# Kernel tuning notes

Hardware: AMD Instinct MI355X
Metric: run time of the kernel (lower is better)

The kernel has to match this reference:

```python
import jax, jax.numpy as jnp
import numpy as np

B, S, D, H = 4, 2048, 1024, 16
DK = D // H
THETA = 10000.0


def _rope(x, pos):
    # x: [..., S, DK]; interleaved-pair rotation as in the torch module
    dk = x.shape[-1]
    inv_freq = 1.0 / (THETA ** (jnp.arange(0, dk, 2, dtype=jnp.float32) / dk))  # [dk/2]
    freqs = pos.astype(jnp.float32)[:, None] * inv_freq  # [S, dk/2]
    cos, sin = jnp.cos(freqs), jnp.sin(freqs)
    xr = x.reshape(*x.shape[:-1], dk // 2, 2)
    x0, x1 = xr[..., 0], xr[..., 1]
    rot = jnp.stack([x0 * cos - x1 * sin, x0 * sin + x1 * cos], axis=-1)
    return rot.reshape(x.shape)


def setup_inputs() -> dict:
    key = jax.random.key(0)
    ks = jax.random.split(key, 5)
    scale = 0.02
    return {
        "x": jax.random.normal(ks[0], (B, S, D), dtype=jnp.float32),
        "Wq": jax.random.normal(ks[1], (D, D), dtype=jnp.float32) * scale,
        "Wk": jax.random.normal(ks[2], (D, D), dtype=jnp.float32) * scale,
        "Wv": jax.random.normal(ks[3], (D, D), dtype=jnp.float32) * scale,
        "Wo": jax.random.normal(ks[4], (D, D), dtype=jnp.float32) * scale,
    }


def reference(x, Wq, Wk, Wv, Wo):
    b, s, d = x.shape
    pos = jnp.arange(s)
    # projections (Linear with no bias, y = x @ W^T)
    q = jnp.einsum('bsd,ed->bse', x, Wq).reshape(b, s, H, DK).transpose(0, 2, 1, 3)
    k = jnp.einsum('bsd,ed->bse', x, Wk).reshape(b, s, H, DK).transpose(0, 2, 1, 3)
    v = jnp.einsum('bsd,ed->bse', x, Wv).reshape(b, s, H, DK).transpose(0, 2, 1, 3)
    q = _rope(q, pos)
    k = _rope(k, pos)
    scores = jnp.einsum('bhqd,bhkd->bhqk', q, k) / jnp.sqrt(jnp.float32(DK))
    causal = jnp.tril(jnp.ones((s, s), dtype=bool))
    scores = jnp.where(causal, scores, -jnp.inf)
    attn = jax.nn.softmax(scores, axis=-1)
    out = jnp.einsum('bhqk,bhkd->bhqd', attn, v)
    out = out.transpose(0, 2, 1, 3).reshape(b, s, d)
    return jnp.einsum('bsd,ed->bse', out, Wo)
```

## Files before the change

kernel.cpp:

```cpp
#include <hip/hip_runtime.h>

#define B_  4
#define S_  2048
#define D_  1024
#define H_  16
#define DK_ 64
#define BH_ (B_*H_)
#define L2E 1.44269504088896f

typedef __attribute__((ext_vector_type(8))) short bf16x8;
typedef __attribute__((ext_vector_type(4))) float f32x4;
typedef __attribute__((ext_vector_type(16))) float f32x16;
typedef __attribute__((ext_vector_type(4))) unsigned u32x4;
typedef unsigned short u16;

__device__ __forceinline__ u16 f2bf(float f){
  unsigned u = __builtin_bit_cast(unsigned, f);
  u += 0x7fffu + ((u >> 16) & 1u);
  return (u16)(u >> 16);
}
__device__ __forceinline__ float bf2f(u16 h){
  unsigned u = ((unsigned)h) << 16;
  return __builtin_bit_cast(float, u);
}

#define GLD16(g,l) __builtin_amdgcn_global_load_lds( \
    (const __attribute__((address_space(1))) void*)(g), \
    (__attribute__((address_space(3))) void*)(l), 16, 0, 0)

#define MFMA16(a,b,c) __builtin_amdgcn_mfma_f32_16x16x32_bf16((a),(b),(c),0,0,0)
#define MFMA32(a,b,c) __builtin_amdgcn_mfma_f32_32x32x16_bf16((a),(b),(c),0,0,0)

__global__ void cast_kernel(const float4* __restrict__ in, ushort4* __restrict__ out, int n4){
  int i = blockIdx.x*blockDim.x + threadIdx.x;
  int stride = gridDim.x*blockDim.x;
  for (; i < n4; i += stride){
    float4 v = in[i];
    ushort4 o;
    o.x = f2bf(v.x); o.y = f2bf(v.y); o.z = f2bf(v.z); o.w = f2bf(v.w);
    out[i] = o;
  }
}

__global__ void cast4_kernel(const float4* __restrict__ w0, const float4* __restrict__ w1,
                             const float4* __restrict__ w2, const float4* __restrict__ w3,
                             ushort4* __restrict__ out){
  const int per = D_*D_/4;
  int i = blockIdx.x*blockDim.x + threadIdx.x;
  int stride = gridDim.x*blockDim.x;
  for (; i < 4*per; i += stride){
    int m = i / per, r = i - m*per;
    const float4* src = (m==0)?w0:(m==1)?w1:(m==2)?w2:w3;
    float4 v = src[r];
    ushort4 o;
    o.x = f2bf(v.x); o.y = f2bf(v.y); o.z = f2bf(v.z); o.w = f2bf(v.w);
    out[i] = o;
  }
}

__global__ void trig_kernel(float* __restrict__ ct, float* __restrict__ st){
  int t = blockIdx.x*blockDim.x + threadIdx.x;
  int i = t & 31, s = t >> 5;
  float expo = -(float)(2*i) * (1.0f/(float)DK_);
  float inv = powf(10000.0f, expo);
  float ang = (float)s * inv;
  ct[t] = cosf(ang);
  st[t] = sinf(ang);
}

template<int MODE>
__global__ __launch_bounds__(256, 2)
void gemm_bt(const u16* __restrict__ A,
             const u16* __restrict__ B0, const u16* __restrict__ B1, const u16* __restrict__ B2,
             u16* __restrict__ O0, u16* __restrict__ O1, u16* __restrict__ O2,
             float* __restrict__ Cf,
             const float* __restrict__ ct, const float* __restrict__ st, int K){
  __shared__ __align__(16) u16 lds[32768];

  const int id = (int)blockIdx.x;
  const int nchunk = (MODE==0) ? 192 : 64;
  const int swz = (id & 7)*nchunk + (id >> 3);
  int z = 0, rem = swz;
  if (MODE == 0){ z = swz >> 9; rem = swz & 511; }
  const int m0 = (rem >> 3) * 128, n0 = (rem & 7) * 128;

  const u16* Bm = B0;
  u16* Om = O0;
  if (MODE == 0){
    if (z == 1){ Bm = B1; Om = O1; }
    else if (z == 2){ Bm = B2; Om = O2; }
  }
  const int tid = threadIdx.x, wave = tid>>6, lane = tid&63;
  const int wm = wave>>1, wn = wave&1;
  const int srow = lane>>3, scol = (lane&7)*8;

  f32x4 acc[4][4];
  #pragma unroll
  for (int m=0;m<4;++m)
    #pragma unroll
    for (int n=0;n<4;++n) acc[m][n] = (f32x4){0.f,0.f,0.f,0.f};

  #define STAGE(kk0,b) { \
    u16* sA = lds + (b)*16384; \
    u16* sB = sA + 8192; \
    _Pragma("unroll") \
    for (int j=0;j<4;++j){ \
      int rb = (wave*4 + j)*8; \
      GLD16(A  + (size_t)(m0 + rb + srow)*K + (kk0) + scol, sA + rb*64); \
      GLD16(Bm + (size_t)(n0 + rb + srow)*K + (kk0) + scol, sB + rb*64); \
    } }

  STAGE(0, 0);
  __syncthreads();

  int cur = 0;
  #pragma unroll 1
  for (int k0 = 0; k0 < K; k0 += 64){
    if (k0 + 64 < K) STAGE(k0 + 64, cur^1);
    const u16* lA = lds + cur*16384;
    const u16* lB = lA + 8192;
    #pragma unroll
    for (int kk=0;kk<2;++kk){
      bf16x8 af[4], bfr[4];
      #pragma unroll
      for (int m=0;m<4;++m) af[m]  = *(const bf16x8*)&lA[(wm*64 + m*16 + (lane&15))*64 + kk*32 + (lane>>4)*8];
      #pragma unroll
      for (int n=0;n<4;++n) bfr[n] = *(const bf16x8*)&lB[(wn*64 + n*16 + (lane&15))*64 + kk*32 + (lane>>4)*8];
      #pragma unroll
      for (int m=0;m<4;++m)
        #pragma unroll
        for (int n=0;n<4;++n)
          acc[m][n] = MFMA16(af[m], bfr[n], acc[m][n]);
    }
    __syncthreads();
    cur ^= 1;
  }
  #undef STAGE

  if (MODE == 0 && z != 2){
    const float scale = (z == 0) ? 0.125f : 1.0f;
    #pragma unroll
    for (int m=0;m<4;++m){
      const int lr0 = wm*64 + m*16 + ((lane>>4)<<2);
      #pragma unroll
      for (int n=0;n<4;++n){
        const int lc = wn*64 + n*16 + (lane&15);
        #pragma unroll
        for (int r=0;r<4;++r){
          const int lr = lr0 + r;
          lds[lr*128 + (lc ^ (((lr>>2)&7)<<4))] = f2bf(acc[m][n][r]);
        }
      }
    }
    __syncthreads();
    #pragma unroll
    for (int k=0;k<8;++k){
      const int cid = k*256 + tid;
      const int rr = cid >> 4, cc = cid & 15;
      bf16x8 v = *(const bf16x8*)&lds[rr*128 + ((cc*8) ^ (((rr>>2)&7)<<4))];
      const int i = m0 + rr, bb = i >> 11, s = i & (S_-1);
      const int e0 = n0 + cc*8, h = e0 >> 6, dk0 = e0 & 63;
      const float4 c4 = *(const float4*)(ct + s*32 + (dk0>>1));
      const float4 s4 = *(const float4*)(st + s*32 + (dk0>>1));
      const float cc4[4] = {c4.x,c4.y,c4.z,c4.w};
      const float ss4[4] = {s4.x,s4.y,s4.z,s4.w};
      bf16x8 o;
      #pragma unroll
      for (int j=0;j<4;++j){
        const float x0 = bf2f((u16)v[2*j]);
        const float x1 = bf2f((u16)v[2*j+1]);
        o[2*j]   = (short)f2bf((x0*cc4[j] - x1*ss4[j])*scale);
        o[2*j+1] = (short)f2bf((x0*ss4[j] + x1*cc4[j])*scale);
      }
      *(bf16x8*)(Om + ((size_t)((bb*H_ + h)*S_ + s))*DK_ + dk0) = o;
    }
  } else {
    #pragma unroll
    for (int m=0;m<4;++m){
      const int rb = m0 + wm*64 + m*16 + ((lane>>4)<<2);
      #pragma unroll
      for (int n=0;n<4;++n){
        const int e = n0 + wn*64 + n*16 + (lane&15);
        if (MODE == 0){
          const int h = e>>6, dk = e&63;
          const int b = rb >> 11, s0 = rb & (S_-1);
          ushort4 w4;
          w4.x = f2bf(acc[m][n][0]); w4.y = f2bf(acc[m][n][1]);
          w4.z = f2bf(acc[m][n][2]); w4.w = f2bf(acc[m][n][3]);
          *(ushort4*)(Om + ((size_t)((b*H_ + h)*DK_ + dk))*S_ + s0) = w4;
        } else {
          #pragma unroll
          for (int r=0;r<4;++r)
            Cf[(size_t)(rb + r)*D_ + e] = acc[m][n][r];
        }
      }
    }
  }
}

__global__ __launch_bounds__(256, 4)
void attn_kernel(const u16* __restrict__ Q, const u16* __restrict__ K,
                 const u16* __restrict__ Vt, u16* __restrict__ O){
  __shared__ __align__(16) u16 lK[2][64*64];
  __shared__ __align__(16) u16 lV[2][64*64];

  const int bh = blockIdx.x;
  const int qt = (int)(gridDim.y - 1 - blockIdx.y);
  const int b = bh >> 4, h = bh & 15;
  const int tid = threadIdx.x, wave = tid>>6, lane = tid&63;
  const int hi = lane >> 5, l31 = lane & 31;
  const int q0 = qt*128, qw = q0 + wave*32;
  const int qg = qw + l31;
  const u16* Qb = Q  + (size_t)bh*S_*DK_;
  const u16* Kb = K  + (size_t)bh*S_*DK_;
  const u16* Vb = Vt + (size_t)bh*DK_*S_;

  bf16x8 qf[4];
  #pragma unroll
  for (int ds=0; ds<4; ++ds)
    qf[ds] = *(const bf16x8*)(Qb + (size_t)qg*DK_ + ds*16 + hi*8);

  f32x16 oacc[2];
  oacc[0] = (f32x16)0.f; oacc[1] = (f32x16)0.f;
  float m_run = -1e30f, l_run = 0.f;

  const int srow8 = lane >> 3;
  const int csw = ((lane&7) ^ srow8) << 3;

  const int kv_end = (qt+1)*128;

  #pragma unroll
  for (int it=0; it<2; ++it){
    const int rb = (it*4 + wave)*8;
    const int row = rb + srow8;
    GLD16(Kb + (size_t)row*DK_ + csw, lK[0] + rb*64);
    GLD16(Vb + (size_t)row*S_ + csw,  lV[0] + rb*64);
  }
  __syncthreads();

  int cur = 0;
  for (int kv0 = 0; kv0 < kv_end; kv0 += 64){
    const int nxt = kv0 + 64;
    if (nxt < kv_end){
      #pragma unroll
      for (int it=0; it<2; ++it){
        const int rb = (it*4 + wave)*8;
        const int row = rb + srow8;
        GLD16(Kb + (size_t)(nxt+row)*DK_ + csw, lK[cur^1] + rb*64);
        GLD16(Vb + (size_t)row*S_ + nxt + csw,  lV[cur^1] + rb*64);
      }
    }

    if (kv0 < qw + 32){
      f32x16 sacc[2];
      sacc[0] = (f32x16)0.f; sacc[1] = (f32x16)0.f;
      __builtin_amdgcn_s_setprio(1);
      #pragma unroll
      for (int kb=0; kb<2; ++kb){
        const int krow = kb*32 + l31;
        #pragma unroll
        for (int ds=0; ds<4; ++ds){
          bf16x8 kf = *(const bf16x8*)&lK[cur][krow*64 + (((ds*2+hi) ^ (krow&7))<<3)];
          sacc[kb] = MFMA32(kf, qf[ds], sacc[kb]);
        }
      }
      __builtin_amdgcn_s_setprio(0);

      if (kv0 + 63 > qw){
        #pragma unroll
        for (int kb=0; kb<2; ++kb)
          #pragma unroll
          for (int r=0; r<16; ++r){
            const int kvg = kv0 + kb*32 + 4*hi + (r&3) + 8*(r>>2);
            if (kvg > qg) sacc[kb][r] = -1e30f;
          }
      }

      float mx = sacc[0][0];
      #pragma unroll
      for (int r=1; r<16; ++r) mx = fmaxf(mx, sacc[0][r]);
      #pragma unroll
      for (int r=0; r<16; ++r) mx = fmaxf(mx, sacc[1][r]);
      mx = fmaxf(mx, __shfl_xor(mx, 32));
      if (!__all((mx - m_run)*L2E <= 8.0f)){
        const float mn = fmaxf(m_run, mx);
        const float alpha = exp2f((m_run - mn)*L2E);
        m_run = mn;
        l_run *= alpha;
        oacc[0] *= alpha;
        oacc[1] *= alpha;
      }
      const float nc = m_run * L2E;
      float ps = 0.f;
      #pragma unroll
      for (int kb=0; kb<2; ++kb)
        #pragma unroll
        for (int r=0; r<16; ++r){
          float v = exp2f(__builtin_fmaf(sacc[kb][r], L2E, -nc));
          sacc[kb][r] = v;
          ps += v;
        }
      ps += __shfl_xor(ps, 32);
      l_run += ps;

      bf16x8 pa[4];
      #pragma unroll
      for (int kb=0; kb<2; ++kb){
        unsigned w[8];
        #pragma unroll
        for (int i=0; i<8; ++i){
          float a = sacc[kb][2*i], b2 = sacc[kb][2*i+1];
          asm("v_cvt_pk_bf16_f32 %0, %1, %2" : "=v"(w[i]) : "v"(a), "v"(b2));
        }
        auto s02 = __builtin_amdgcn_permlane32_swap(w[0], w[2], false, false);
        auto s13 = __builtin_amdgcn_permlane32_swap(w[1], w[3], false, false);
        auto s46 = __builtin_amdgcn_permlane32_swap(w[4], w[6], false, false);
        auto s57 = __builtin_amdgcn_permlane32_swap(w[5], w[7], false, false);
        u32x4 ua = {s02[0], s13[0], s02[1], s13[1]};
        u32x4 ub = {s46[0], s57[0], s46[1], s57[1]};
        pa[kb*2+0] = __builtin_bit_cast(bf16x8, ua);
        pa[kb*2+1] = __builtin_bit_cast(bf16x8, ub);
      }

      __builtin_amdgcn_s_setprio(1);
      #pragma unroll
      for (int dkb=0; dkb<2; ++dkb){
        const int vrow = dkb*32 + l31;
        #pragma unroll
        for (int ks=0; ks<4; ++ks){
          bf16x8 vf = *(const bf16x8*)&lV[cur][vrow*64 + (((ks*2+hi) ^ (vrow&7))<<3)];
          oacc[dkb] = MFMA32(vf, pa[ks], oacc[dkb]);
        }
      }
      __builtin_amdgcn_s_setprio(0);
    }
    __syncthreads();
    cur ^= 1;
  }

  const float inv = 1.0f / l_run;
  #pragma unroll
  for (int dkb=0; dkb<2; ++dkb)
    #pragma unroll
    for (int rq=0; rq<4; ++rq){
      ushort4 w4;
      w4.x = f2bf(oacc[dkb][rq*4+0]*inv);
      w4.y = f2bf(oacc[dkb][rq*4+1]*inv);
      w4.z = f2bf(oacc[dkb][rq*4+2]*inv);
      w4.w = f2bf(oacc[dkb][rq*4+3]*inv);
      const int dk0 = dkb*32 + 8*rq + 4*hi;
      *(ushort4*)(O + (size_t)(b*S_+qg)*D_ + h*DK_ + dk0) = w4;
    }
}

extern "C" void kernel_launch(void* const* d_in, const int* in_sizes, int n_in,
                              void* d_out, int out_size, void* d_ws, size_t ws_size,
                              hipStream_t stream){
  const float* x  = (const float*)d_in[0];
  const float* Wq = (const float*)d_in[1];
  const float* Wk = (const float*)d_in[2];
  const float* Wv = (const float*)d_in[3];
  const float* Wo = (const float*)d_in[4];
  float* out = (float*)d_out;
  char* ws = (char*)d_ws;

  size_t off = 0;
  u16* xb  = (u16*)(ws + off); off += (size_t)B_*S_*D_*2;
  u16* wqb = (u16*)(ws + off); off += (size_t)D_*D_*2;
  u16* wkb = (u16*)(ws + off); off += (size_t)D_*D_*2;
  u16* wvb = (u16*)(ws + off); off += (size_t)D_*D_*2;
  u16* wob = (u16*)(ws + off); off += (size_t)D_*D_*2;
  u16* Qb  = (u16*)(ws + off); off += (size_t)BH_*S_*DK_*2;
  u16* Kb  = (u16*)(ws + off); off += (size_t)BH_*S_*DK_*2;
  u16* Vtb = (u16*)(ws + off); off += (size_t)BH_*S_*DK_*2;
  u16* Ob  = (u16*)(ws + off); off += (size_t)B_*S_*D_*2;
  float* ct = (float*)(ws + off); off += (size_t)S_*32*4;
  float* st = (float*)(ws + off); off += (size_t)S_*32*4;

  cast_kernel<<<2048,256,0,stream>>>((const float4*)x,  (ushort4*)xb,  B_*S_*D_/4);
  cast4_kernel<<<1024,256,0,stream>>>((const float4*)Wq, (const float4*)Wk,
                                      (const float4*)Wv, (const float4*)Wo, (ushort4*)wqb);
  trig_kernel<<<(S_*32)/256,256,0,stream>>>(ct, st);

  gemm_bt<0><<<1536,256,0,stream>>>(xb, wqb,wkb,wvb, Qb,Kb,Vtb, nullptr, ct, st, D_);

  attn_kernel<<<dim3(BH_, S_/128),256,0,stream>>>(Qb, Kb, Vtb, Ob);

  gemm_bt<1><<<512,256,0,stream>>>(Ob, wob,wob,wob, nullptr,nullptr,nullptr, out, nullptr, nullptr, D_);
}
```

Measured before the change: 185.0 us.

## Use 256x256-tile 8-wave QKV GEMM with quarter-step LDS pipelining

Replaces the QKV projection GEMM with a dedicated 512-thread kernel that computes 256x256 output tiles. It splits each K-step into four quadrant MFMA phases, interleaving global-to-LDS staging with explicit barriers, waitcnts and priority hints, and uses an XOR-swizzled LDS layout. The goal is more data reuse per tile, fewer LDS bank conflicts, and load latency hidden behind MFMA work. In exchange it uses 128KB of LDS and a large accumulator set, which lowers occupancy, and it adds a hand-tuned synchronisation scheme. The output GEMM is split into its own non-templated kernel.

```diff
diff --git a/kernel.cpp b/kernel.cpp
--- a/kernel.cpp
+++ b/kernel.cpp
@@ -30,6 +30,11 @@
 
 #define MFMA16(a,b,c) __builtin_amdgcn_mfma_f32_16x16x32_bf16((a),(b),(c),0,0,0)
 #define MFMA32(a,b,c) __builtin_amdgcn_mfma_f32_32x32x16_bf16((a),(b),(c),0,0,0)
+
+#define BARR() __builtin_amdgcn_s_barrier()
+#define LGKM0() do { asm volatile("s_waitcnt lgkmcnt(0)" ::: "memory"); \
+                     __builtin_amdgcn_sched_barrier(0); } while(0)
+#define VMW(N) asm volatile("s_waitcnt vmcnt(" #N ")" ::: "memory")
 
 __global__ void cast_kernel(const float4* __restrict__ in, ushort4* __restrict__ out, int n4){
   int i = blockIdx.x*blockDim.x + threadIdx.x;
@@ -68,28 +73,191 @@
   st[t] = sinf(ang);
 }
 
-template<int MODE>
+__global__ __launch_bounds__(512, 2)
+void gemm_qkv8(const u16* __restrict__ A,
+               const u16* __restrict__ B0m, const u16* __restrict__ B1m, const u16* __restrict__ B2m,
+               u16* __restrict__ O0, u16* __restrict__ O1, u16* __restrict__ O2,
+               const float* __restrict__ ct, const float* __restrict__ st){
+  __shared__ __align__(16) u16 lds[65536];
+
+  const int id = (int)blockIdx.x;
+  const int swz = (id & 7)*48 + (id >> 3);
+  const int z = swz >> 7;
+  const int rem = swz & 127;
+  const int m0 = (rem >> 2)*256, n0 = (rem & 3)*256;
+
+  const u16* Bm = (z==0) ? B0m : (z==1) ? B1m : B2m;
+  u16* Om = (z==0) ? O0 : (z==1) ? O1 : O2;
+
+  const int tid = threadIdx.x, wave = tid>>6, lane = tid&63;
+  const int wm = wave>>2, wn = wave&3;
+  const int l15 = lane & 15, l4 = lane >> 4;
+  const int srow8 = lane >> 3;
+  const int csw = ((lane&7) ^ srow8) << 3;
+
+  f32x4 acc[8][4];
+  #pragma unroll
+  for (int mi=0;mi<8;++mi)
+    #pragma unroll
+    for (int ni=0;ni<4;++ni) acc[mi][ni] = (f32x4){0.f,0.f,0.f,0.f};
+
+  #define STAGE_A(pp, mh, kc) do { \
+    u16* base_ = lds + (pp) + (mh)*8192; \
+    _Pragma("unroll") \
+    for (int j_=0;j_<2;++j_){ \
+      const int lr_ = (wave*2 + j_)*8; \
+      const int q_ = lr_ >> 6; \
+      const size_t grow_ = (size_t)(m0 + q_*128 + (mh)*64 + (lr_ & 63) + srow8); \
+      GLD16(A + grow_*1024 + (kc) + csw, base_ + lr_*64); \
+    } } while(0)
+
+  #define STAGE_B(pp, nh, kc) do { \
+    u16* base_ = lds + (pp) + 16384 + (nh)*8192; \
+    _Pragma("unroll") \
+    for (int j_=0;j_<2;++j_){ \
+      const int lr_ = (wave*2 + j_)*8; \
+      const int sub_ = lr_ >> 5; \
+      const size_t grow_ = (size_t)(n0 + sub_*64 + (nh)*32 + (lr_ & 31) + srow8); \
+      GLD16(Bm + grow_*1024 + (kc) + csw, base_ + lr_*64); \
+    } } while(0)
+
+  bf16x8 af[4][2], bfr[2][2];
+  #define LOAD_AF(pp, mh) do { \
+    const u16* ab_ = lds + (pp) + (mh)*8192; \
+    _Pragma("unroll") \
+    for (int m_=0;m_<4;++m_) \
+      _Pragma("unroll") \
+      for (int kk_=0;kk_<2;++kk_){ \
+        const int lr_ = wm*64 + m_*16 + l15; \
+        af[m_][kk_] = *(const bf16x8*)&ab_[lr_*64 + (((kk_*4 + l4) ^ (lr_&7))<<3)]; \
+      } } while(0)
+
+  #define LOAD_BF(pp, nh) do { \
+    const u16* bb_ = lds + (pp) + 16384 + (nh)*8192; \
+    _Pragma("unroll") \
+    for (int n_=0;n_<2;++n_) \
+      _Pragma("unroll") \
+      for (int kk_=0;kk_<2;++kk_){ \
+        const int lr_ = wn*32 + n_*16 + l15; \
+        bfr[n_][kk_] = *(const bf16x8*)&bb_[lr_*64 + (((kk_*4 + l4) ^ (lr_&7))<<3)]; \
+      } } while(0)
+
+  #define MFMAQ(mh, nh) do { \
+    _Pragma("unroll") \
+    for (int m_=0;m_<4;++m_) \
+      _Pragma("unroll") \
+      for (int n_=0;n_<2;++n_) \
+        _Pragma("unroll") \
+        for (int kk_=0;kk_<2;++kk_) \
+          acc[(mh)*4+m_][(nh)*2+n_] = MFMA16(af[m_][kk_], bfr[n_][kk_], acc[(mh)*4+m_][(nh)*2+n_]); \
+    } while(0)
+
+  STAGE_A(0, 0, 0); STAGE_A(0, 1, 0); STAGE_B(0, 0, 0); STAGE_B(0, 1, 0);
+  STAGE_B(32768, 0, 64); STAGE_A(32768, 1, 64);
+  VMW(4);
+  BARR();
+
+  #pragma unroll 1
+  for (int t = 0; t < 16; ++t){
+    const int p = (t & 1) << 15;
+    const int o = p ^ 32768;
+    const int kc1 = ((t+1 < 16) ? t+1 : 15)*64;
+    const int kc2 = ((t+2 < 16) ? t+2 : 15)*64;
+    LOAD_AF(p, 0); LOAD_BF(p, 0);
+    STAGE_A(o, 0, kc1);
+    BARR(); LGKM0();
+    __builtin_amdgcn_s_setprio(1); MFMAQ(0, 0); __builtin_amdgcn_s_setprio(0);
+    BARR();
+    LOAD_AF(p, 1);
+    STAGE_B(o, 1, kc1);
+    BARR(); LGKM0();
+    __builtin_amdgcn_s_setprio(1); MFMAQ(1, 0); __builtin_amdgcn_s_setprio(0);
+    BARR();
+    LOAD_BF(p, 1);
+    STAGE_B(p, 0, kc2);
+    BARR(); LGKM0();
+    __builtin_amdgcn_s_setprio(1); MFMAQ(1, 1); __builtin_amdgcn_s_setprio(0);
+    BARR();
+    LOAD_AF(p, 0);
+    STAGE_A(p, 1, kc2);
+    BARR(); LGKM0();
+    __builtin_amdgcn_s_setprio(1); MFMAQ(0, 1); __builtin_amdgcn_s_setprio(0);
+    VMW(4);
+    BARR();
+  }
+  #undef STAGE_A
+  #undef STAGE_B
+  #undef LOAD_AF
+  #undef LOAD_BF
+  #undef MFMAQ
+
+  VMW(0);
+  BARR();
+
+  if (z != 2){
+    const float scale = (z == 0) ? 0.125f : 1.0f;
+    #pragma unroll
+    for (int mi=0;mi<8;++mi){
+      const int rr0 = wm*128 + (mi>>2)*64 + (mi&3)*16 + l4*4;
+      #pragma unroll
+      for (int ni=0;ni<4;++ni){
+        const int cc = wn*64 + (ni>>1)*32 + (ni&1)*16 + l15;
+        #pragma unroll
+        for (int r=0;r<4;++r){
+          const int rr = rr0 + r;
+          lds[rr*256 + (((((cc>>3) ^ (rr&7)))<<3) | (cc&7))] = f2bf(acc[mi][ni][r]);
+        }
+      }
+    }
+    __syncthreads();
+    #pragma unroll
+    for (int k=0;k<16;++k){
+      const int cid = k*512 + tid;
+      const int rr = cid >> 5, cc8 = cid & 31;
+      bf16x8 v = *(const bf16x8*)&lds[rr*256 + ((cc8 ^ (rr&7))<<3)];
+      const int i = m0 + rr, bb = i >> 11, s = i & (S_-1);
+      const int e0 = n0 + cc8*8, h = e0 >> 6, dk0 = e0 & 63;
+      const float4 c4 = *(const float4*)(ct + s*32 + (dk0>>1));
+      const float4 s4 = *(const float4*)(st + s*32 + (dk0>>1));
+      const float cc4[4] = {c4.x,c4.y,c4.z,c4.w};
+      const float ss4[4] = {s4.x,s4.y,s4.z,s4.w};
+      bf16x8 o;
+      #pragma unroll
+      for (int j=0;j<4;++j){
+        const float x0 = bf2f((u16)v[2*j]);
+        const float x1 = bf2f((u16)v[2*j+1]);
+        o[2*j]   = (short)f2bf((x0*cc4[j] - x1*ss4[j])*scale);
+        o[2*j+1] = (short)f2bf((x0*ss4[j] + x1*cc4[j])*scale);
+      }
+      *(bf16x8*)(Om + ((size_t)((bb*H_ + h)*S_ + s))*DK_ + dk0) = o;
+    }
+  } else {
+    #pragma unroll
+    for (int mi=0;mi<8;++mi){
+      const int rb = m0 + wm*128 + (mi>>2)*64 + (mi&3)*16 + l4*4;
+      const int b = rb >> 11, s0 = rb & (S_-1);
+      #pragma unroll
+      for (int ni=0;ni<4;++ni){
+        const int e = n0 + wn*64 + (ni>>1)*32 + (ni&1)*16 + l15;
+        const int h = e>>6, dk = e&63;
+        ushort4 w4;
+        w4.x = f2bf(acc[mi][ni][0]); w4.y = f2bf(acc[mi][ni][1]);
+        w4.z = f2bf(acc[mi][ni][2]); w4.w = f2bf(acc[mi][ni][3]);
+        *(ushort4*)(Om + ((size_t)((b*H_ + h)*DK_ + dk))*S_ + s0) = w4;
+      }
+    }
+  }
+}
+
 __global__ __launch_bounds__(256, 2)
-void gemm_bt(const u16* __restrict__ A,
-             const u16* __restrict__ B0, const u16* __restrict__ B1, const u16* __restrict__ B2,
-             u16* __restrict__ O0, u16* __restrict__ O1, u16* __restrict__ O2,
-             float* __restrict__ Cf,
-             const float* __restrict__ ct, const float* __restrict__ st, int K){
+void gemm_out(const u16* __restrict__ A, const u16* __restrict__ Bw,
+              float* __restrict__ Cf){
   __shared__ __align__(16) u16 lds[32768];
 
   const int id = (int)blockIdx.x;
-  const int nchunk = (MODE==0) ? 192 : 64;
-  const int swz = (id & 7)*nchunk + (id >> 3);
-  int z = 0, rem = swz;
-  if (MODE == 0){ z = swz >> 9; rem = swz & 511; }
-  const int m0 = (rem >> 3) * 128, n0 = (rem & 7) * 128;
-
-  const u16* Bm = B0;
-  u16* Om = O0;
-  if (MODE == 0){
-    if (z == 1){ Bm = B1; Om = O1; }
-    else if (z == 2){ Bm = B2; Om = O2; }
-  }
+  const int swz = (id & 7)*64 + (id >> 3);
+  const int m0 = (swz >> 3) * 128, n0 = (swz & 7) * 128;
+
   const int tid = threadIdx.x, wave = tid>>6, lane = tid&63;
   const int wm = wave>>1, wn = wave&1;
   const int srow = lane>>3, scol = (lane&7)*8;
@@ -106,8 +274,8 @@
     _Pragma("unroll") \
     for (int j=0;j<4;++j){ \
       int rb = (wave*4 + j)*8; \
-      GLD16(A  + (size_t)(m0 + rb + srow)*K + (kk0) + scol, sA + rb*64); \
-      GLD16(Bm + (size_t)(n0 + rb + srow)*K + (kk0) + scol, sB + rb*64); \
+      GLD16(A  + (size_t)(m0 + rb + srow)*D_ + (kk0) + scol, sA + rb*64); \
+      GLD16(Bw + (size_t)(n0 + rb + srow)*D_ + (kk0) + scol, sB + rb*64); \
     } }
 
   STAGE(0, 0);
@@ -115,8 +283,8 @@
 
   int cur = 0;
   #pragma unroll 1
-  for (int k0 = 0; k0 < K; k0 += 64){
-    if (k0 + 64 < K) STAGE(k0 + 64, cur^1);
+  for (int k0 = 0; k0 < D_; k0 += 64){
+    if (k0 + 64 < D_) STAGE(k0 + 64, cur^1);
     const u16* lA = lds + cur*16384;
     const u16* lB = lA + 8192;
     #pragma unroll
@@ -137,63 +305,15 @@
   }
   #undef STAGE
 
-  if (MODE == 0 && z != 2){
-    const float scale = (z == 0) ? 0.125f : 1.0f;
-    #pragma unroll
-    for (int m=0;m<4;++m){
-      const int lr0 = wm*64 + m*16 + ((lane>>4)<<2);
-      #pragma unroll
-      for (int n=0;n<4;++n){
-        const int lc = wn*64 + n*16 + (lane&15);
-        #pragma unroll
-        for (int r=0;r<4;++r){
-          const int lr = lr0 + r;
-          lds[lr*128 + (lc ^ (((lr>>2)&7)<<4))] = f2bf(acc[m][n][r]);
-        }
-      }
-    }
-    __syncthreads();
-    #pragma unroll
-    for (int k=0;k<8;++k){
-      const int cid = k*256 + tid;
-      const int rr = cid >> 4, cc = cid & 15;
-      bf16x8 v = *(const bf16x8*)&lds[rr*128 + ((cc*8) ^ (((rr>>2)&7)<<4))];
-      const int i = m0 + rr, bb = i >> 11, s = i & (S_-1);
-      const int e0 = n0 + cc*8, h = e0 >> 6, dk0 = e0 & 63;
-      const float4 c4 = *(const float4*)(ct + s*32 + (dk0>>1));
-      const float4 s4 = *(const float4*)(st + s*32 + (dk0>>1));
-      const float cc4[4] = {c4.x,c4.y,c4.z,c4.w};
-      const float ss4[4] = {s4.x,s4.y,s4.z,s4.w};
-      bf16x8 o;
-      #pragma unroll
-      for (int j=0;j<4;++j){
-        const float x0 = bf2f((u16)v[2*j]);
-        const float x1 = bf2f((u16)v[2*j+1]);
-        o[2*j]   = (short)f2bf((x0*cc4[j] - x1*ss4[j])*scale);
-        o[2*j+1] = (short)f2bf((x0*ss4[j] + x1*cc4[j])*scale);
-      }
-      *(bf16x8*)(Om + ((size_t)((bb*H_ + h)*S_ + s))*DK_ + dk0) = o;
-    }
-  } else {
-    #pragma unroll
-    for (int m=0;m<4;++m){
-      const int rb = m0 + wm*64 + m*16 + ((lane>>4)<<2);
-      #pragma unroll
-      for (int n=0;n<4;++n){
-        const int e = n0 + wn*64 + n*16 + (lane&15);
-        if (MODE == 0){
-          const int h = e>>6, dk = e&63;
-          const int b = rb >> 11, s0 = rb & (S_-1);
-          ushort4 w4;
-          w4.x = f2bf(acc[m][n][0]); w4.y = f2bf(acc[m][n][1]);
-          w4.z = f2bf(acc[m][n][2]); w4.w = f2bf(acc[m][n][3]);
-          *(ushort4*)(Om + ((size_t)((b*H_ + h)*DK_ + dk))*S_ + s0) = w4;
-        } else {
-          #pragma unroll
-          for (int r=0;r<4;++r)
-            Cf[(size_t)(rb + r)*D_ + e] = acc[m][n][r];
-        }
-      }
+  #pragma unroll
+  for (int m=0;m<4;++m){
+    const int rb = m0 + wm*64 + m*16 + ((lane>>4)<<2);
+    #pragma unroll
+    for (int n=0;n<4;++n){
+      const int e = n0 + wn*64 + n*16 + (lane&15);
+      #pragma unroll
+      for (int r=0;r<4;++r)
+        Cf[(size_t)(rb + r)*D_ + e] = acc[m][n][r];
     }
   }
 }
@@ -382,9 +502,9 @@
                                       (const float4*)Wv, (const float4*)Wo, (ushort4*)wqb);
   trig_kernel<<<(S_*32)/256,256,0,stream>>>(ct, st);
 
-  gemm_bt<0><<<1536,256,0,stream>>>(xb, wqb,wkb,wvb, Qb,Kb,Vtb, nullptr, ct, st, D_);
+  gemm_qkv8<<<384,512,0,stream>>>(xb, wqb,wkb,wvb, Qb,Kb,Vtb, ct, st);
 
   attn_kernel<<<dim3(BH_, S_/128),256,0,stream>>>(Qb, Kb, Vtb, Ob);
 
-  gemm_bt<1><<<512,256,0,stream>>>(Ob, wob,wob,wob, nullptr,nullptr,nullptr, out, nullptr, nullptr, D_);
-}
+  gemm_out<<<512,256,0,stream>>>(Ob, wob, out);
+}
```

Result: no change. 188.5 us (+1.9%).
